# Performance work log

Measured on AMD Instinct MI355X. Metric: run time of the kernel, lower is better.

The kernel has to match this reference:

```python
import jax, jax.numpy as jnp
import numpy as np

EMBED_DIM = 768
NUM_HEADS = 12
HEAD_DIM = EMBED_DIM // NUM_HEADS
WINDOW = 64
B, S = 2, 2048


def setup_inputs() -> dict:
    key = jax.random.key(0)
    ks = jax.random.split(key, 8)
    xavier = 0.1 * np.sqrt(6.0 / (EMBED_DIM + EMBED_DIM))  # xavier_uniform with gain=0.1
    def lin_w(k):
        return jax.random.uniform(k, (EMBED_DIM, EMBED_DIM), jnp.float32, -xavier, xavier)
    return {
        "query": jax.random.normal(ks[0], (B, S, EMBED_DIM), jnp.float32),
        "key": jax.random.normal(ks[1], (B, S, EMBED_DIM), jnp.float32),
        "value": jax.random.normal(ks[2], (B, S, EMBED_DIM), jnp.float32),
        "key_padding_mask": jnp.zeros((B, S), dtype=bool),
        "Wq": lin_w(ks[3]), "bq": jnp.zeros((EMBED_DIM,), jnp.float32),
        "Wk": lin_w(ks[4]), "bk": jnp.zeros((EMBED_DIM,), jnp.float32),
        "Wv": lin_w(ks[5]), "bv": jnp.zeros((EMBED_DIM,), jnp.float32),
        "Wo": lin_w(ks[6]), "bo": jnp.zeros((EMBED_DIM,), jnp.float32),
    }


def reference(query, key, value, key_padding_mask, Wq, bq, Wk, bk, Wv, bv, Wo, bo):
    Bsz, Sl, E = query.shape
    H, D = NUM_HEADS, HEAD_DIM

    def proj(x, W, b):  # nn.Linear: x @ W.T + b, then split heads -> [B,H,S,D]
        return (x @ W.T + b).reshape(Bsz, Sl, H, D).transpose(0, 2, 1, 3)

    q = proj(query, Wq, bq)
    k = proj(key, Wk, bk)
    v = proj(value, Wv, bv)

    scale = float(D) ** -0.5
    scores = jnp.einsum("bhqd,bhkd->bhqk", q, k) * scale  # [B,H,S,S]

    idx = jnp.arange(Sl)
    win_mask = jnp.abs(idx[:, None] - idx[None, :]) > WINDOW  # True = masked out
    scores = jnp.where(win_mask[None, None], -10000.0, scores)
    scores = jnp.where(key_padding_mask[:, None, None, :], -10000.0, scores)
    scores = jnp.where(jnp.isnan(scores), -10000.0, scores)

    attn = jax.nn.softmax(scores, axis=-1) + 1e-6
    attn = jnp.where(jnp.isnan(attn), 1.0 / Sl, attn)

    ctx = jnp.einsum("bhqk,bhkd->bhqd", attn, v)
    ctx = ctx.transpose(0, 2, 1, 3).reshape(Bsz, Sl, E)
    out = ctx @ Wo.T + bo
    out = jnp.where(jnp.isnan(out), value, out)
    return out, attn
```

## Files before the change

### kernel.cpp

```cpp
#include <hip/hip_runtime.h>
#include <hip/hip_bf16.h>

#define EMBED 768
#define NHEADS 12
#define HDIM 64
#define WIN 64
#define BATCH 2
#define SEQ 2048
#define MROWS (BATCH*SEQ)
#define NBH (BATCH*NHEADS)
#define QT 32
#define KP 160
#define KPAD 168
#define SPAD 164

typedef __attribute__((ext_vector_type(8))) short short8;
typedef __attribute__((ext_vector_type(4))) float f32x4;

__device__ __forceinline__ float bf2f(unsigned short u) {
    union { unsigned int i; float f; } z;
    z.i = ((unsigned int)u) << 16;
    return z.f;
}
__device__ __forceinline__ unsigned short f2bf(float f) {
    __hip_bfloat16 h = __float2bfloat16(f);
    return *reinterpret_cast<unsigned short*>(&h);
}

__device__ __forceinline__ void gload16(const void* g, void* l) {
    __builtin_amdgcn_global_load_lds(
        (const __attribute__((address_space(1))) unsigned int*)g,
        (__attribute__((address_space(3))) unsigned int*)l,
        16, 0, 0);
}

struct CvtArgs {
    const float* src[4];
    unsigned short* dst[4];
};

__global__ __launch_bounds__(256) void cvt_w(CvtArgs ca) {
    const int n4 = EMBED * EMBED / 4;
    const int bper = (n4 + 255) / 256;
    int seg = blockIdx.x / bper;
    int i = (blockIdx.x - seg * bper) * 256 + threadIdx.x;
    if (i < n4) {
        float4 v = reinterpret_cast<const float4*>(ca.src[seg])[i];
        ushort4 o;
        o.x = f2bf(v.x); o.y = f2bf(v.y); o.z = f2bf(v.z); o.w = f2bf(v.w);
        reinterpret_cast<ushort4*>(ca.dst[seg])[i] = o;
    }
}

struct GArgs {
    const void* A[3];
    const unsigned short* Bm[3];
    const float* bias[3];
    void* C[3];
};

template<int F32OUT, int F32A>
__global__ __launch_bounds__(256) void gemm_nt(GArgs ga, int M, int N, int K) {
    const int NPANEL = gridDim.y * gridDim.z;
    const int flat = (blockIdx.z * gridDim.y + blockIdx.y) * gridDim.x + blockIdx.x;
    const int xcd = flat & 7;
    const int j = flat >> 3;
    const int panel = xcd * (NPANEL >> 3) + j / gridDim.x;
    const int z = panel / gridDim.y;
    const int bm = (panel % gridDim.y) * 128;
    const int bn = (j % gridDim.x) * 128;

    const unsigned short* __restrict__ Bm = ga.Bm[z];
    const float* __restrict__ bias = ga.bias[z];

    __shared__ alignas(16) unsigned char AsRaw[F32A ? 128 * 32 * 4 : 128 * 32 * 2];
    __shared__ unsigned short Bs[128 * 32];

    const int tid = threadIdx.x;
    const int lane = tid & 63;
    const int wid = tid >> 6;
    const int wm = wid >> 1, wn = wid & 1;

    f32x4 acc[4][4] = {};

    const int fr = lane & 15;
    const int krow = (lane >> 4) * 8;

    for (int k0 = 0; k0 < K; k0 += 32) {
        if (F32A) {
            const float* Af = (const float*)ga.A[z];
            float* AsF = (float*)AsRaw;
#pragma unroll
            for (int it = 0; it < 4; ++it) {
                int idx = it * 256 + tid;
                int r = idx >> 3;
                int cc = idx & 7;
                int gcc = cc ^ (r & 7);
                gload16(Af + (size_t)(bm + r) * K + k0 + gcc * 4, &AsF[idx * 4]);
            }
        } else {
            const unsigned short* Ab = (const unsigned short*)ga.A[z];
#pragma unroll
            for (int it = 0; it < 2; ++it) {
                int idx = it * 256 + tid;
                int r = idx >> 2;
                int c = (idx & 3) * 8;
                gload16(Ab + (size_t)(bm + r) * K + k0 + c,
                        (unsigned short*)AsRaw + idx * 8);
            }
        }
#pragma unroll
        for (int it = 0; it < 2; ++it) {
            int idx = it * 256 + tid;
            int r = idx >> 2;
            int c = (idx & 3) * 8;
            gload16(Bm + (size_t)(bn + r) * K + k0 + c, &Bs[idx * 8]);
        }
        __syncthreads();

        short8 af[4], bfv[4];
#pragma unroll
        for (int mf = 0; mf < 4; ++mf) {
            int r = wm * 64 + mf * 16 + fr;
            if (F32A) {
                const float* AsF = (const float*)AsRaw;
                int kc0 = (lane >> 4) * 2;
                int s0 = kc0 ^ (r & 7);
                f32x4 v0 = *reinterpret_cast<const f32x4*>(&AsF[(r * 8 + s0) * 4]);
                f32x4 v1 = *reinterpret_cast<const f32x4*>(&AsF[(r * 8 + (s0 ^ 1)) * 4]);
                unsigned short* ou = reinterpret_cast<unsigned short*>(&af[mf]);
                ou[0] = f2bf(v0[0]); ou[1] = f2bf(v0[1]);
                ou[2] = f2bf(v0[2]); ou[3] = f2bf(v0[3]);
                ou[4] = f2bf(v1[0]); ou[5] = f2bf(v1[1]);
                ou[6] = f2bf(v1[2]); ou[7] = f2bf(v1[3]);
            } else {
                af[mf] = *reinterpret_cast<const short8*>(
                    (const unsigned short*)AsRaw + r * 32 + krow);
            }
        }
#pragma unroll
        for (int nf = 0; nf < 4; ++nf)
            bfv[nf] = *reinterpret_cast<const short8*>(&Bs[(wn * 64 + nf * 16 + fr) * 32 + krow]);
#pragma unroll
        for (int mf = 0; mf < 4; ++mf)
#pragma unroll
            for (int nf = 0; nf < 4; ++nf)
                acc[mf][nf] = __builtin_amdgcn_mfma_f32_16x16x32_bf16(
                    af[mf], bfv[nf], acc[mf][nf], 0, 0, 0);
        __syncthreads();
    }

    const int fq = lane >> 4;
#pragma unroll
    for (int mf = 0; mf < 4; ++mf)
#pragma unroll
        for (int nf = 0; nf < 4; ++nf) {
            int col = bn + wn * 64 + nf * 16 + fr;
            float bv = bias[col];
#pragma unroll
            for (int r = 0; r < 4; ++r) {
                int row = bm + wm * 64 + mf * 16 + fq * 4 + r;
                float v = acc[mf][nf][r] + bv;
                if (F32OUT)
                    reinterpret_cast<float*>(ga.C[z])[(size_t)row * N + col] = v;
                else
                    reinterpret_cast<unsigned short*>(ga.C[z])[(size_t)row * N + col] = f2bf(v);
            }
        }
}

__global__ __launch_bounds__(256) void sumv_kernel(const unsigned short* __restrict__ Vb,
                                                   float* __restrict__ sumV) {
    __shared__ float r[32][HDIM];
    const int bh = blockIdx.x;
    const int b = bh / NHEADS, h = bh % NHEADS;
    const int dg = (threadIdx.x & 7) * 8;
    const int r0 = threadIdx.x >> 3;
    float acc[8] = {};
    const unsigned short* vp = Vb + (size_t)(b * SEQ) * EMBED + h * HDIM + dg;
    for (int j = r0; j < SEQ; j += 32) {
        short8 v = *reinterpret_cast<const short8*>(vp + (size_t)j * EMBED);
#pragma unroll
        for (int e = 0; e < 8; ++e)
            acc[e] += bf2f(((const unsigned short*)&v)[e]);
    }
#pragma unroll
    for (int e = 0; e < 8; ++e) r[r0][dg + e] = acc[e];
    __syncthreads();
    if (threadIdx.x < HDIM) {
        float s = 0.f;
#pragma unroll
        for (int i = 0; i < 32; ++i) s += r[i][threadIdx.x];
        sumV[bh * HDIM + threadIdx.x] = s;
    }
}

__global__ __launch_bounds__(256, 3) void attn_mfma(
    const unsigned short* __restrict__ Q,
    const unsigned short* __restrict__ Kb,
    const unsigned short* __restrict__ Vb,
    const unsigned char* __restrict__ kpm,
    const float* __restrict__ sumV,
    float* __restrict__ attn_out,
    unsigned short* __restrict__ ctx) {
    const int flat = blockIdx.y * gridDim.x + blockIdx.x;
    const int g2 = (flat & 7) * 192 + (flat >> 3);
    const int bh = g2 >> 6;
    const int qt = g2 & 63;
    const int h = bh % NHEADS;
    const int b = bh / NHEADS;
    const int q0 = qt * QT;
    const int kstart = max(q0 - WIN, 0);

    __shared__ float Sf[QT][SPAD];
    __shared__ unsigned short Pb[QT][KPAD];
    __shared__ unsigned short Vt[HDIM][KPAD];

    const int tid = threadIdx.x;
    const int l = tid & 63;
    const int w = tid >> 6;
    const int fr = l & 15;
    const int ksl = (l >> 4) * 8;

    const size_t base = (size_t)(b * SEQ) * EMBED + h * HDIM;

    const int nfb = (w & 1) * 2;
    const float sv0 = 1e-6f * sumV[bh * HDIM + nfb * 16 + fr];
    const float sv1 = 1e-6f * sumV[bh * HDIM + (nfb + 1) * 16 + fr];

    {
        const int mf = w >> 1;
        const int nt0 = (w & 1) * 5;

        const unsigned short* qrow = Q + base + (size_t)(q0 + mf * 16 + fr) * EMBED;
        short8 aq0 = *reinterpret_cast<const short8*>(qrow + ksl);
        short8 aq1 = *reinterpret_cast<const short8*>(qrow + 32 + ksl);

        f32x4 sacc[5] = {};
#pragma unroll
        for (int t = 0; t < 5; ++t) {
            int jg = kstart + (nt0 + t) * 16 + fr;
            int jc = min(jg, SEQ - 1);
            const unsigned short* krow = Kb + base + (size_t)jc * EMBED;
            short8 b0 = *reinterpret_cast<const short8*>(krow + ksl);
            short8 b1 = *reinterpret_cast<const short8*>(krow + 32 + ksl);
            sacc[t] = __builtin_amdgcn_mfma_f32_16x16x32_bf16(aq0, b0, sacc[t], 0, 0, 0);
            sacc[t] = __builtin_amdgcn_mfma_f32_16x16x32_bf16(aq1, b1, sacc[t], 0, 0, 0);
        }

#pragma unroll
        for (int t = 0; t < 5; ++t) {
            int col = (nt0 + t) * 16 + fr;
            int jg = kstart + col;
            bool jvalid = (jg < SEQ);
            bool mk = jvalid && kpm[b * SEQ + jg];
#pragma unroll
            for (int r = 0; r < 4; ++r) {
                int rowl = mf * 16 + (l >> 4) * 4 + r;
                int qi = q0 + rowl;
                float s = sacc[t][r] * 0.125f;
                if (mk) s = -10000.f;
                int dd = qi - jg;
                if (!jvalid || dd > WIN || dd < -WIN) s = -1e30f;
                Sf[rowl][col] = s;
            }
        }

#pragma unroll
        for (int pass = 0; pass < 5; ++pass) {
            int jrel = pass * 32 + (tid >> 3);
            int jg = kstart + jrel;
            int dg = (tid & 7) * 8;
            short8 v = {};
            if (jg < SEQ)
                v = *reinterpret_cast<const short8*>(Vb + base + (size_t)jg * EMBED + dg);
#pragma unroll
            for (int e = 0; e < 8; ++e)
                Vt[dg + e][jrel] = ((const unsigned short*)&v)[e];
        }
    }
    __syncthreads();

    {
        const int row = tid >> 3;
        const int cg = tid & 7;
        float e[KP / 8];
        float m = -1e30f;
#pragma unroll
        for (int i = 0; i < KP / 8; ++i) {
            float s = Sf[row][cg + i * 8];
            e[i] = s;
            m = fmaxf(m, s);
        }
#pragma unroll
        for (int off = 1; off < 8; off <<= 1) m = fmaxf(m, __shfl_xor(m, off));
        float sum = 0.f;
#pragma unroll
        for (int i = 0; i < KP / 8; ++i) {
            e[i] = __expf(e[i] - m);
            sum += e[i];
        }
#pragma unroll
        for (int off = 1; off < 8; off <<= 1) sum += __shfl_xor(sum, off);
        float inv = 1.f / sum;
#pragma unroll
        for (int i = 0; i < KP / 8; ++i) {
            float p = e[i] * inv;
            int col = cg + i * 8;
            Sf[row][col] = p;
            Pb[row][col] = f2bf(p);
        }
    }
    __syncthreads();

    {
        const f32x4 fill = {1e-6f, 1e-6f, 1e-6f, 1e-6f};
#pragma unroll
        for (int rr = 0; rr < QT / 4; ++rr) {
            int row = w * (QT / 4) + rr;
            int qi = q0 + row;
            int blo = max(qi - WIN, 0);
            int bhi = min(qi + WIN, SEQ - 1);
            float* __restrict__ orow = attn_out + ((size_t)bh * SEQ + qi) * SEQ;
#pragma unroll
            for (int seg = 0; seg < SEQ / 256; ++seg) {
                if (seg * 256 + 255 >= blo && seg * 256 <= bhi) continue;
                __builtin_nontemporal_store(
                    fill, reinterpret_cast<f32x4*>(orow + seg * 256 + l * 4));
            }
        }
    }

    {
#pragma unroll
        for (int rr = 0; rr < QT / 4; ++rr) {
            int row = w * (QT / 4) + rr;
            int qi = q0 + row;
            int blo = max(qi - WIN, 0);
            int bhi = min(qi + WIN, SEQ - 1);
            float* __restrict__ orow = attn_out + ((size_t)bh * SEQ + qi) * SEQ;
            int slo = blo >> 8;
            int shi = bhi >> 8;
            for (int seg = slo; seg <= shi; ++seg) {
                int c0 = seg * 256 + l * 4;
                f32x4 v = {1e-6f, 1e-6f, 1e-6f, 1e-6f};
#pragma unroll
                for (int e = 0; e < 4; ++e) {
                    int c = c0 + e;
                    if (c >= blo && c <= bhi) v[e] = Sf[row][c - kstart] + 1e-6f;
                }
                __builtin_nontemporal_store(v, reinterpret_cast<f32x4*>(orow + c0));
            }
        }
    }

    {
        const int mf = w >> 1;
        f32x4 oacc[2] = {};
#pragma unroll
        for (int kk = 0; kk < KP / 32; ++kk) {
            short8 a = *reinterpret_cast<const short8*>(&Pb[mf * 16 + fr][kk * 32 + ksl]);
#pragma unroll
            for (int n2 = 0; n2 < 2; ++n2) {
                short8 bv = *reinterpret_cast<const short8*>(&Vt[(nfb + n2) * 16 + fr][kk * 32 + ksl]);
                oacc[n2] = __builtin_amdgcn_mfma_f32_16x16x32_bf16(a, bv, oacc[n2], 0, 0, 0);
            }
        }
#pragma unroll
        for (int n2 = 0; n2 < 2; ++n2) {
            int d = (nfb + n2) * 16 + fr;
            float sv = (n2 == 0) ? sv0 : sv1;
#pragma unroll
            for (int r = 0; r < 4; ++r) {
                int rowl = mf * 16 + (l >> 4) * 4 + r;
                ctx[base + (size_t)(q0 + rowl) * EMBED + d] = f2bf(oacc[n2][r] + sv);
            }
        }
    }
}

extern "C" void kernel_launch(void* const* d_in, const int* in_sizes, int n_in,
                              void* d_out, int out_size, void* d_ws, size_t ws_size,
                              hipStream_t stream) {
    const float* q_in = (const float*)d_in[0];
    const float* k_in = (const float*)d_in[1];
    const float* v_in = (const float*)d_in[2];
    const unsigned char* kpm = (const unsigned char*)d_in[3];
    const float* Wq = (const float*)d_in[4];
    const float* bq = (const float*)d_in[5];
    const float* Wk = (const float*)d_in[6];
    const float* bk = (const float*)d_in[7];
    const float* Wv = (const float*)d_in[8];
    const float* bv = (const float*)d_in[9];
    const float* Wo = (const float*)d_in[10];
    const float* bo = (const float*)d_in[11];

    char* ws = (char*)d_ws;
    size_t off = 0;
    auto alloc = [&](size_t bytes) {
        void* p = ws + off;
        off += (bytes + 255) & ~255ULL;
        return p;
    };
    const size_t XB = (size_t)MROWS * EMBED * 2;
    const size_t WB = (size_t)EMBED * EMBED * 2;
    unsigned short* wqb = (unsigned short*)alloc(WB);
    unsigned short* wkb = (unsigned short*)alloc(WB);
    unsigned short* wvb = (unsigned short*)alloc(WB);
    unsigned short* wob = (unsigned short*)alloc(WB);
    unsigned short* Qb = (unsigned short*)alloc(XB);
    unsigned short* Kb = (unsigned short*)alloc(XB);
    unsigned short* Vb = (unsigned short*)alloc(XB);
    unsigned short* ctx = (unsigned short*)alloc(XB);
    float* sumV = (float*)alloc((size_t)NBH * HDIM * 4);

    float* out0 = (float*)d_out;
    float* attn_out = out0 + (size_t)MROWS * EMBED;

    {
        CvtArgs ca;
        ca.src[0] = Wq; ca.src[1] = Wk; ca.src[2] = Wv; ca.src[3] = Wo;
        ca.dst[0] = wqb; ca.dst[1] = wkb; ca.dst[2] = wvb; ca.dst[3] = wob;
        int bper = (EMBED * EMBED / 4 + 255) / 256;
        cvt_w<<<dim3(4 * bper), dim3(256), 0, stream>>>(ca);
    }

    {
        GArgs ga;
        ga.A[0] = q_in; ga.A[1] = k_in; ga.A[2] = v_in;
        ga.Bm[0] = wqb; ga.Bm[1] = wkb; ga.Bm[2] = wvb;
        ga.bias[0] = bq; ga.bias[1] = bk; ga.bias[2] = bv;
        ga.C[0] = Qb; ga.C[1] = Kb; ga.C[2] = Vb;
        gemm_nt<0, 1><<<dim3(EMBED / 128, MROWS / 128, 3), dim3(256), 0, stream>>>(
            ga, MROWS, EMBED, EMBED);
    }

    sumv_kernel<<<dim3(NBH), dim3(256), 0, stream>>>(Vb, sumV);

    attn_mfma<<<dim3(SEQ / QT, NBH), dim3(256), 0, stream>>>(
        Qb, Kb, Vb, kpm, sumV, attn_out, ctx);

    {
        GArgs ga;
        ga.A[0] = ctx;  ga.A[1] = ctx;  ga.A[2] = ctx;
        ga.Bm[0] = wob; ga.Bm[1] = wob; ga.Bm[2] = wob;
        ga.bias[0] = bo; ga.bias[1] = bo; ga.bias[2] = bo;
        ga.C[0] = out0; ga.C[1] = out0; ga.C[2] = out0;
        gemm_nt<1, 0><<<dim3(EMBED / 128, MROWS / 128, 1), dim3(256), 0, stream>>>(
            ga, MROWS, EMBED, EMBED);
    }
}
```

Measured before the change: 164.8 us.

## Move attention-matrix constant fill into weight-conversion kernel

The constant 1e-6 fill of the off-window attention entries moves out of the attention kernel and into the weight-conversion kernel. That kernel now grid-strides over the whole attention output with nontemporal stores, and the attention kernel later overwrites the in-window segments. The aim is to take the large fill store traffic off the attention kernel's critical path, at the cost of writing the full matrix, including window segments that get rewritten. The conversion kernel uses only a few thousand blocks, so the fill loop runs many iterations per thread.

```diff
diff --git a/kernel.cpp b/kernel.cpp
--- a/kernel.cpp
+++ b/kernel.cpp
@@ -37,19 +37,26 @@
 struct CvtArgs {
     const float* src[4];
     unsigned short* dst[4];
+    float* fill;
 };
 
-__global__ __launch_bounds__(256) void cvt_w(CvtArgs ca) {
+__global__ __launch_bounds__(256) void cvt_fill(CvtArgs ca) {
     const int n4 = EMBED * EMBED / 4;
     const int bper = (n4 + 255) / 256;
     int seg = blockIdx.x / bper;
     int i = (blockIdx.x - seg * bper) * 256 + threadIdx.x;
-    if (i < n4) {
+    if (seg < 4 && i < n4) {
         float4 v = reinterpret_cast<const float4*>(ca.src[seg])[i];
         ushort4 o;
         o.x = f2bf(v.x); o.y = f2bf(v.y); o.z = f2bf(v.z); o.w = f2bf(v.w);
         reinterpret_cast<ushort4*>(ca.dst[seg])[i] = o;
     }
+    const size_t FILLN = (size_t)NBH * SEQ * (SEQ / 4);
+    const size_t nthreads = (size_t)gridDim.x * 256;
+    const f32x4 fv = {1e-6f, 1e-6f, 1e-6f, 1e-6f};
+    f32x4* p = reinterpret_cast<f32x4*>(ca.fill);
+    for (size_t idx = (size_t)blockIdx.x * 256 + threadIdx.x; idx < FILLN; idx += nthreads)
+        __builtin_nontemporal_store(fv, p + idx);
 }
 
 struct GArgs {
@@ -312,24 +319,6 @@
         }
     }
     __syncthreads();
-
-    {
-        const f32x4 fill = {1e-6f, 1e-6f, 1e-6f, 1e-6f};
-#pragma unroll
-        for (int rr = 0; rr < QT / 4; ++rr) {
-            int row = w * (QT / 4) + rr;
-            int qi = q0 + row;
-            int blo = max(qi - WIN, 0);
-            int bhi = min(qi + WIN, SEQ - 1);
-            float* __restrict__ orow = attn_out + ((size_t)bh * SEQ + qi) * SEQ;
-#pragma unroll
-            for (int seg = 0; seg < SEQ / 256; ++seg) {
-                if (seg * 256 + 255 >= blo && seg * 256 <= bhi) continue;
-                __builtin_nontemporal_store(
-                    fill, reinterpret_cast<f32x4*>(orow + seg * 256 + l * 4));
-            }
-        }
-    }
 
     {
 #pragma unroll
@@ -421,8 +410,9 @@
         CvtArgs ca;
         ca.src[0] = Wq; ca.src[1] = Wk; ca.src[2] = Wv; ca.src[3] = Wo;
         ca.dst[0] = wqb; ca.dst[1] = wkb; ca.dst[2] = wvb; ca.dst[3] = wob;
+        ca.fill = attn_out;
         int bper = (EMBED * EMBED / 4 + 255) / 256;
-        cvt_w<<<dim3(4 * bper), dim3(256), 0, stream>>>(ca);
+        cvt_fill<<<dim3(4 * bper), dim3(256), 0, stream>>>(ca);
     }
 
     {
```

Result: slower. 182.7 us (+10.9%).
